# Kernel tuning notes

Measured on AMD Instinct MI355X. Metric: run time of the kernel, lower is better.

The kernel has to match this reference:

```python
import jax, jax.numpy as jnp
import numpy as np

# Config (matches init_kwargs): range [-32,32]^3, voxel 0.5 -> 128^3 grid; BEV 200x200
PC_LOW = np.array([-32.0, -32.0, -32.0], dtype=np.float32)
PC_HIGH = np.array([32.0, 32.0, 32.0], dtype=np.float32)
VOX = 0.5
G = 128
BEV_H, BEV_W = 200, 200
BN_EPS = 1e-5
STRIDES = [1, 2, 1, 2, 1, 1]


def setup_inputs() -> dict:
    key = jax.random.key(0)
    ks = jax.random.split(key, 10)
    N = 2_000_000
    xyz = jax.random.uniform(ks[0], (N, 3), jnp.float32, minval=-32.0, maxval=32.0)
    inten = jax.random.uniform(ks[1], (N, 1), jnp.float32)
    points = jnp.concatenate([xyz, inten], axis=1)  # (N,4)
    chans = [(32, 4), (64, 32), (64, 64), (128, 64), (128, 128), (256, 128)]
    inp = {"points": points}
    for i, (co, ci) in enumerate(chans):
        fan_in = ci * 27
        inp[f"w{i+1}"] = jax.random.normal(ks[2 + i], (co, ci, 3, 3, 3), jnp.float32) / np.sqrt(fan_in)
        inp[f"g{i+1}"] = jnp.ones((co,), jnp.float32)
        inp[f"b{i+1}"] = jnp.zeros((co,), jnp.float32)
    return inp


def _voxelize(points):
    # range filtering + floor-binning + clamp, faithful to voxelize_points (dense path: scatter-ADD)
    low = jnp.asarray(PC_LOW)
    high = jnp.asarray(PC_HIGH)
    mask = jnp.all((points[:, :3] >= low) & (points[:, :3] <= high), axis=1)
    coords = jnp.floor((points[:, :3] - low) / VOX).astype(jnp.int32)
    coords = jnp.clip(coords, 0, G - 1)
    vals = points * mask[:, None].astype(points.dtype)  # invalid points contribute 0
    # original indexes voxel_grid[:, z, y, x]
    grid = jnp.zeros((G, G, G, 4), points.dtype)
    grid = grid.at[coords[:, 2], coords[:, 1], coords[:, 0]].add(vals)
    return jnp.transpose(grid, (3, 0, 1, 2))  # (4, G, G, G)


def _conv3d(x, w, s):
    # PyTorch Conv3d(k=3, padding=1, stride=s), NCDHW
    return jax.lax.conv_general_dilated(
        x, w, window_strides=(s, s, s), padding=[(1, 1), (1, 1), (1, 1)],
        dimension_numbers=("NCDHW", "OIDHW", "NCDHW"))


def _bn_relu(x, g, b):
    # eval-mode BN: running_mean=0, running_var=1
    scale = (g / jnp.sqrt(1.0 + BN_EPS))[None, :, None, None, None]
    return jax.nn.relu(x * scale + b[None, :, None, None, None])


def reference(points, w1, w2, w3, w4, w5, w6,
              g1, g2, g3, g4, g5, g6,
              b1, b2, b3, b4, b5, b6):
    ws = [w1, w2, w3, w4, w5, w6]
    gs = [g1, g2, g3, g4, g5, g6]
    bs = [b1, b2, b3, b4, b5, b6]
    x = _voxelize(points)[None]  # (1,4,G,G,G)
    for w, g, b, s in zip(ws, gs, bs, STRIDES):
        x = _bn_relu(_conv3d(x, w, s), g, b)
    feat = x[0]  # (256, G/4, G/4, G/4)
    bev = jnp.max(feat, axis=2)  # torch.max(..., dim=2) on (C,D1,D2,D3) -> (C,D1,D3)
    # F.interpolate bilinear align_corners=False == jax.image.resize half-pixel bilinear
    bev = jax.image.resize(bev, (bev.shape[0], BEV_H, BEV_W), method="bilinear")
    return bev
```

## Files before the change

### kernel.cpp

```cpp
#include <hip/hip_runtime.h>
#include <hip/hip_fp16.h>
#include <cstdint>
#include <cstddef>

typedef __attribute__((ext_vector_type(8))) short short8;
typedef __attribute__((ext_vector_type(8))) _Float16 half8;
typedef __attribute__((ext_vector_type(16))) float f32x16;

__device__ __forceinline__ float bf2f(unsigned short u) { return __uint_as_float(((unsigned)u) << 16); }
__device__ __forceinline__ unsigned short f2bf(float f) {
    unsigned u = __float_as_uint(f);
    return (unsigned short)((u + 0x7fffu + ((u >> 16) & 1u)) >> 16);
}
__device__ __forceinline__ void sync_lds() {
    asm volatile("s_waitcnt lgkmcnt(0)\n\ts_barrier" ::: "memory");
}

static constexpr float BN_INV = 0.9999950000374997f;

__global__ __launch_bounds__(256) void voxelize_kernel(const float4* __restrict__ pts,
                                                       __half2* __restrict__ grid, int N) {
    int i = blockIdx.x * 256 + threadIdx.x;
    if (i >= N) return;
    float4 p = pts[i];
    if (p.x < -32.f || p.x > 32.f || p.y < -32.f || p.y > 32.f || p.z < -32.f || p.z > 32.f) return;
    int cx = min(max((int)floorf((p.x + 32.f) * 2.f), 0), 127);
    int cy = min(max((int)floorf((p.y + 32.f) * 2.f), 0), 127);
    int cz = min(max((int)floorf((p.z + 32.f) * 2.f), 0), 127);
    int idx = ((((cz + 1) * 130) + (cy + 1)) * 130 + (cx + 1)) * 2;
    unsafeAtomicAdd(&grid[idx],     __floats2half2_rn(p.x, p.y));
    unsafeAtomicAdd(&grid[idx + 1], __floats2half2_rn(p.z, p.w));
}

__global__ __launch_bounds__(256) void repack_w(const float* __restrict__ w, const float* __restrict__ g,
                                                unsigned short* __restrict__ o, int Co, int CI) {
    int i = blockIdx.x * 256 + threadIdx.x;
    int total = 27 * Co * CI;
    if (i >= total) return;
    int ci = i % CI;
    int t = i / CI;
    int co = t % Co;
    int k = t / Co;
    float v = w[((size_t)(co * CI + ci)) * 27 + k] * g[co] * BN_INV;
    o[i] = f2bf(v);
}
__global__ __launch_bounds__(256) void repack_w1m(const float* __restrict__ w, const float* __restrict__ g,
                                                  unsigned short* __restrict__ o) {
    int i = blockIdx.x * 256 + threadIdx.x;
    if (i >= 9 * 32 * 16) return;
    int k16 = i & 15;
    int co = (i >> 4) & 31;
    int p = i >> 9;
    float v = 0.f;
    if (k16 < 12) {
        int dx = k16 >> 2, ci = k16 & 3;
        int dz = p / 3, dy = p % 3;
        v = w[(co * 4 + ci) * 27 + dz * 9 + dy * 3 + dx] * g[co] * BN_INV;
    }
    o[i] = __half_as_ushort(__float2half(v));
}

__global__ __launch_bounds__(256) void conv1_mfma(
    const unsigned short* __restrict__ in, const unsigned short* __restrict__ wa,
    const float* __restrict__ beta, unsigned short* __restrict__ out,
    int zstart, int r0) {
    const int tid = threadIdx.x;
    const int l31 = tid & 31;
    const int lh = (tid >> 5) & 1;
    const int wv = tid >> 6;
    int v = blockIdx.x * 128 + wv * 32 + l31;
    int x = v & 127;
    int y = (v >> 7) & 127;
    int z = zstart + (v >> 14);

    const unsigned short* base = in + ((z * 130 + y) * 130 + x) * 4 + lh * 8;
    uint2 d0[9], d1[9];
    half8 a[9];
#pragma unroll
    for (int p = 0; p < 9; ++p) {
        int dz = p / 3, dy = p % 3;
        const unsigned short* rp = base + (dz * 130 + dy) * 520;
        d0[p] = *(const uint2*)(rp);
        d1[p] = *(const uint2*)(rp + 4);
        a[p] = *(const half8*)(wa + (p * 32 + l31) * 16 + lh * 8);
    }
    f32x16 acc = {0.f};
#pragma unroll
    for (int p = 0; p < 9; ++p) {
        uint4 braw = {d0[p].x, d0[p].y, d1[p].x, d1[p].y};
        half8 b = *(half8*)&braw;
        acc = __builtin_amdgcn_mfma_f32_32x32x16_f16(a[p], b, acc, 0, 0, 0);
    }
    int r = z - zstart + r0;
    int ob = ((r * 130 + (y + 1)) * 130 + (x + 1)) * 32;
#pragma unroll
    for (int g = 0; g < 4; ++g) {
        int cb = 4 * lh + 8 * g;
        float4 bt = *(const float4*)(beta + cb);
        ushort4 u;
        u.x = f2bf(fmaxf(acc[g * 4 + 0] + bt.x, 0.f));
        u.y = f2bf(fmaxf(acc[g * 4 + 1] + bt.y, 0.f));
        u.z = f2bf(fmaxf(acc[g * 4 + 2] + bt.z, 0.f));
        u.w = f2bf(fmaxf(acc[g * 4 + 3] + bt.w, 0.f));
        *(ushort4*)(out + ob + cb) = u;
    }
}

template <int CI, int KC, int S>
__global__ __launch_bounds__(256) void conv_mfma(
    const unsigned short* __restrict__ in, const unsigned short* __restrict__ wb,
    const float* __restrict__ beta, unsigned short* __restrict__ out,
    int D, int lgD, int Xp, int Xpo, int Co, int zin_base, int v_off) {

    constexpr int KCp = KC + 8;
    constexpr int OPB = KC / 8;
    constexpr int NB = KC / 16;
    constexpr int NA = KC / 32;
    constexpr int NCH = KC / 16;
    constexpr int NCC = CI / KC;
    constexpr int STOT = 27 * NCC;

    __shared__ __align__(16) short sA[2 * 64 * KCp];
    __shared__ __align__(16) short sB[2 * 128 * KCp];

    const int tid = threadIdx.x;
    const int l31 = tid & 31;
    const int lh = (tid >> 5) & 1;
    const int wv = tid >> 6;
    const int co0 = blockIdx.x * 64;

    int bgIdx[NB], blB[NB];
#pragma unroll
    for (int j = 0; j < NB; ++j) {
        int idx = tid + j * 256;
        int vL = idx / OPB;
        int oct = idx - vL * OPB;
        int vg = v_off + blockIdx.y * 128 + vL;
        int x = vg & (D - 1);
        int ry = vg >> lgD;
        int y = ry & (D - 1);
        int z = ry >> lgD;
        bgIdx[j] = ((z * S * Xp + y * S) * Xp + x * S) * CI + oct * 8;
        blB[j] = vL * KCp + oct * 8;
    }
    int agIdx[NA], alA[NA];
#pragma unroll
    for (int j = 0; j < NA; ++j) {
        int idx = tid + j * 256;
        int cA = idx / OPB;
        int oct = idx - cA * OPB;
        agIdx[j] = (co0 + cA) * CI + oct * 8;
        alA[j] = cA * KCp + oct * 8;
    }
    const int bfr = (wv * 32 + l31) * KCp + lh * 8;
    const int afr = l31 * KCp + lh * 8;

    short8 rB[2][NB], rA[2][NA];

    auto loadStage = [&](int s, int r) {
        int k = s / NCC;
        int c0 = (s - k * NCC) * KC;
        int dz = k / 9;
        int rr = k - dz * 9;
        int dy = rr / 3;
        int dx = rr - dy * 3;
        int kb = (((dz - zin_base) * Xp + dy) * Xp + dx) * CI + c0;
        int ka = k * Co * CI + c0;
#pragma unroll
        for (int j = 0; j < NB; ++j) rB[r][j] = *(const short8*)(in + bgIdx[j] + kb);
#pragma unroll
        for (int j = 0; j < NA; ++j) rA[r][j] = *(const short8*)(wb + agIdx[j] + ka);
    };
    auto storeLDS = [&](int r, int buf) {
#pragma unroll
        for (int j = 0; j < NB; ++j) *(short8*)(sB + buf * 128 * KCp + blB[j]) = rB[r][j];
#pragma unroll
        for (int j = 0; j < NA; ++j) *(short8*)(sA + buf * 64 * KCp + alA[j]) = rA[r][j];
    };

    f32x16 acc0 = {0.f}, acc1 = {0.f};

    loadStage(0, 0);
    loadStage(1, 1);
    storeLDS(0, 0);
    sync_lds();

#pragma unroll
    for (int s = 0; s < STOT; ++s) {
        if (s + 2 < STOT) loadStage(s + 2, s & 1);
        const short* pB = sB + (s & 1) * 128 * KCp + bfr;
        const short* pA = sA + (s & 1) * 64 * KCp + afr;
#pragma unroll
        for (int c = 0; c < NCH; ++c) {
            short8 bv = *(const short8*)(pB + c * 16);
            short8 a0 = *(const short8*)(pA + c * 16);
            short8 a1 = *(const short8*)(pA + 32 * KCp + c * 16);
            acc0 = __builtin_amdgcn_mfma_f32_32x32x16_bf16(a0, bv, acc0, 0, 0, 0);
            acc1 = __builtin_amdgcn_mfma_f32_32x32x16_bf16(a1, bv, acc1, 0, 0, 0);
        }
        if (s + 1 < STOT) {
            storeLDS((s + 1) & 1, (s + 1) & 1);
            sync_lds();
        }
    }

    int vg = v_off + blockIdx.y * 128 + wv * 32 + l31;
    int x = vg & (D - 1);
    int ry = vg >> lgD;
    int y = ry & (D - 1);
    int z = ry >> lgD;
    size_t ob = (((size_t)(z + 1) * Xpo + (y + 1)) * Xpo + (x + 1)) * Co + co0;
#pragma unroll
    for (int cot = 0; cot < 2; ++cot) {
        const f32x16& a = cot ? acc1 : acc0;
#pragma unroll
        for (int g = 0; g < 4; ++g) {
            int cb = cot * 32 + 4 * lh + 8 * g;
            float4 bt = *(const float4*)(beta + co0 + cb);
            ushort4 u;
            u.x = f2bf(fmaxf(a[g * 4 + 0] + bt.x, 0.f));
            u.y = f2bf(fmaxf(a[g * 4 + 1] + bt.y, 0.f));
            u.z = f2bf(fmaxf(a[g * 4 + 2] + bt.z, 0.f));
            u.w = f2bf(fmaxf(a[g * 4 + 3] + bt.w, 0.f));
            *(ushort4*)(out + ob + cb) = u;
        }
    }
}

__global__ __launch_bounds__(256) void bev_max_kernel(const unsigned short* __restrict__ feat,
                                                      float* __restrict__ bev) {
    int z = blockIdx.x >> 5;
    int x = blockIdx.x & 31;
    int c = threadIdx.x;
    const unsigned short* p = feat + ((((z + 1) * 34) + 1) * 34 + (x + 1)) * 256 + c;
    float mx = 0.f;
#pragma unroll
    for (int y = 0; y < 32; ++y) mx = fmaxf(mx, bf2f(p[y * 34 * 256]));
    bev[(z * 32 + x) * 256 + c] = mx;
}

__global__ __launch_bounds__(256) void resize_kernel(const float* __restrict__ bev,
                                                     float* __restrict__ out) {
    int i = blockIdx.x * 256 + threadIdx.x;
    if (i >= 256 * 200 * 200) return;
    int ox = i % 200;
    int t = i / 200;
    int oy = t % 200;
    int c = t / 200;
    const float sc = 32.0f / 200.0f;
    float fy = (oy + 0.5f) * sc - 0.5f;
    float fx = (ox + 0.5f) * sc - 0.5f;
    float fy0 = floorf(fy), fx0 = floorf(fx);
    float ty = fy - fy0, tx = fx - fx0;
    int y0 = min(max((int)fy0, 0), 31), y1 = min(max((int)fy0 + 1, 0), 31);
    int x0 = min(max((int)fx0, 0), 31), x1 = min(max((int)fx0 + 1, 0), 31);
    float v00 = bev[(y0 * 32 + x0) * 256 + c], v01 = bev[(y0 * 32 + x1) * 256 + c];
    float v10 = bev[(y1 * 32 + x0) * 256 + c], v11 = bev[(y1 * 32 + x1) * 256 + c];
    float top = v00 + tx * (v01 - v00);
    float bot = v10 + tx * (v11 - v10);
    out[i] = top + ty * (bot - top);
}

extern "C" void kernel_launch(void* const* d_in, const int* in_sizes, int n_in,
                              void* d_out, int out_size, void* d_ws, size_t ws_size,
                              hipStream_t stream) {
    const float* points = (const float*)d_in[0];
    int N = in_sizes[0] / 4;
    const float *W[6], *G[6], *B[6];
    for (int i = 0; i < 6; ++i) {
        W[i] = (const float*)d_in[1 + 3 * i];
        G[i] = (const float*)d_in[2 + 3 * i];
        B[i] = (const float*)d_in[3 + 3 * i];
    }

    char* ws = (char*)d_ws;
    const size_t MiB = 1ull << 20;
    unsigned short* gridH = (unsigned short*)(ws);
    unsigned short* O1s = (unsigned short*)(ws + 18 * MiB);
    unsigned short* O2p = (unsigned short*)(ws + 104 * MiB);
    unsigned short* O3p = (unsigned short*)(ws);
    unsigned short* O4p = (unsigned short*)(ws + 37 * MiB);
    unsigned short* O5p = (unsigned short*)(ws + 48 * MiB);
    unsigned short* O6p = (unsigned short*)(ws + 59 * MiB);
    float* bev = (float*)(ws + 80 * MiB);
    unsigned short* wc1 = (unsigned short*)(ws + 140 * MiB);
    unsigned short* wb2 = (unsigned short*)(ws + 140 * MiB + 16384);
    unsigned short* wb3 = wb2 + 27 * 64 * 32;
    unsigned short* wb4 = wb3 + 27 * 64 * 64;
    unsigned short* wb5 = wb4 + 27 * 128 * 64;
    unsigned short* wb6 = wb5 + 27 * 128 * 128;

    repack_w1m<<<18, 256, 0, stream>>>(W[0], G[0], wc1);
    repack_w<<<216, 256, 0, stream>>>(W[1], G[1], wb2, 64, 32);
    repack_w<<<432, 256, 0, stream>>>(W[2], G[2], wb3, 64, 64);
    repack_w<<<864, 256, 0, stream>>>(W[3], G[3], wb4, 128, 64);
    repack_w<<<1728, 256, 0, stream>>>(W[4], G[4], wb5, 128, 128);
    repack_w<<<3456, 256, 0, stream>>>(W[5], G[5], wb6, 256, 128);

    hipMemsetAsync(gridH, 0, 17576000, stream);
    hipMemsetAsync(O2p, 0, 36799488, stream);
    voxelize_kernel<<<(N + 255) / 256, 256, 0, stream>>>((const float4*)points, (__half2*)gridH, N);

    hipMemsetAsync(O1s, 0, 70304000, stream);
    conv1_mfma<<<8192, 256, 0, stream>>>(gridH, wc1, B[0], O1s, 0, 1);
    conv_mfma<32, 32, 2><<<dim3(1, 1024), 256, 0, stream>>>(O1s, wb2, B[1], O2p, 64, 6, 130, 66, 64, 0, 0);
    conv1_mfma<<<8320, 256, 0, stream>>>(gridH, wc1, B[0], O1s, 63, 0);
    conv_mfma<32, 32, 2><<<dim3(1, 1024), 256, 0, stream>>>(O1s, wb2, B[1], O2p, 64, 6, 130, 66, 64, 64, 131072);

    hipMemsetAsync(O3p, 0, 36799488, stream);
    hipMemsetAsync(O4p, 0, 10061824, stream);
    hipMemsetAsync(O5p, 0, 10061824, stream);
    hipMemsetAsync(O6p, 0, 20123648, stream);

    conv_mfma<64, 64, 1><<<dim3(1, 2048), 256, 0, stream>>>(O2p, wb3, B[2], O3p, 64, 6, 66, 66, 64, 0, 0);
    conv_mfma<64, 64, 2><<<dim3(2, 256), 256, 0, stream>>>(O3p, wb4, B[3], O4p, 32, 5, 66, 34, 128, 0, 0);
    conv_mfma<128, 64, 1><<<dim3(2, 256), 256, 0, stream>>>(O4p, wb5, B[4], O5p, 32, 5, 34, 34, 128, 0, 0);
    conv_mfma<128, 64, 1><<<dim3(4, 256), 256, 0, stream>>>(O5p, wb6, B[5], O6p, 32, 5, 34, 34, 256, 0, 0);

    bev_max_kernel<<<1024, 256, 0, stream>>>(O6p, bev);
    resize_kernel<<<40000, 256, 0, stream>>>(bev, (float*)d_out);
}
```

Before: 763.5 us.

## Replace global atomic voxelization with bucket sort and LDS accumulation

Voxelization now runs as four steps: count points per (z, y-quarter) bucket, prefix-scan the counts, scatter the points into bucket order, then accumulate each bucket in fp32 in LDS and write fp16 results to the grid. This removes 4M global fp16 atomics spread across a 17 MB grid and replaces them with LDS atomics plus coalesced writes. In exchange it reads the points twice, writes and reads a 32 MB sorted buffer, and adds kernel launches. The fp32 accumulation also changes rounding compared with the fp16 atomic sums.

```diff
diff --git a/kernel.cpp b/kernel.cpp
--- a/kernel.cpp
+++ b/kernel.cpp
@@ -18,18 +18,114 @@
 
 static constexpr float BN_INV = 0.9999950000374997f;
 
-__global__ __launch_bounds__(256) void voxelize_kernel(const float4* __restrict__ pts,
-                                                       __half2* __restrict__ grid, int N) {
-    int i = blockIdx.x * 256 + threadIdx.x;
-    if (i >= N) return;
-    float4 p = pts[i];
-    if (p.x < -32.f || p.x > 32.f || p.y < -32.f || p.y > 32.f || p.z < -32.f || p.z > 32.f) return;
-    int cx = min(max((int)floorf((p.x + 32.f) * 2.f), 0), 127);
+
+__device__ __forceinline__ int vox_bucket(float4 p, bool& ok) {
+    ok = !(p.x < -32.f || p.x > 32.f || p.y < -32.f || p.y > 32.f || p.z < -32.f || p.z > 32.f);
     int cy = min(max((int)floorf((p.y + 32.f) * 2.f), 0), 127);
     int cz = min(max((int)floorf((p.z + 32.f) * 2.f), 0), 127);
-    int idx = ((((cz + 1) * 130) + (cy + 1)) * 130 + (cx + 1)) * 2;
-    unsafeAtomicAdd(&grid[idx],     __floats2half2_rn(p.x, p.y));
-    unsafeAtomicAdd(&grid[idx + 1], __floats2half2_rn(p.z, p.w));
+    return cz * 4 + (cy >> 5);
+}
+
+__global__ __launch_bounds__(256) void vox_count(const float4* __restrict__ pts,
+                                                 int* __restrict__ cnt, int N) {
+    __shared__ int h[512];
+    for (int t = threadIdx.x; t < 512; t += 256) h[t] = 0;
+    __syncthreads();
+    int stride = gridDim.x * 256;
+    for (int i = blockIdx.x * 256 + threadIdx.x; i < N; i += stride) {
+        float4 p = pts[i];
+        bool ok;
+        int bk = vox_bucket(p, ok);
+        if (ok) atomicAdd(&h[bk], 1);
+    }
+    __syncthreads();
+    for (int t = threadIdx.x; t < 512; t += 256)
+        if (h[t]) atomicAdd(&cnt[t], h[t]);
+}
+
+__global__ void vox_scan(const int* __restrict__ cnt, int* __restrict__ off,
+                         int* __restrict__ cur) {
+    __shared__ int c[512];
+    int t = threadIdx.x;
+    c[t] = cnt[t];
+    __syncthreads();
+    int s = 0;
+    for (int i = 0; i < t; ++i) s += c[i];
+    off[t] = s;
+    cur[t] = s;
+}
+
+__global__ __launch_bounds__(256) void vox_scatter(const float4* __restrict__ pts,
+                                                   int* __restrict__ cur,
+                                                   float4* __restrict__ sorted, int N) {
+    __shared__ int h[512];
+    __shared__ int base[512];
+    int b0 = blockIdx.x * 4096;
+    for (int t = threadIdx.x; t < 512; t += 256) h[t] = 0;
+    __syncthreads();
+    float4 p[16];
+    int bk[16];
+#pragma unroll
+    for (int j = 0; j < 16; ++j) {
+        int i = b0 + j * 256 + threadIdx.x;
+        bk[j] = -1;
+        if (i < N) {
+            p[j] = pts[i];
+            bool ok;
+            int b = vox_bucket(p[j], ok);
+            if (ok) {
+                bk[j] = b;
+                atomicAdd(&h[b], 1);
+            }
+        }
+    }
+    __syncthreads();
+    for (int t = threadIdx.x; t < 512; t += 256) {
+        int n = h[t];
+        base[t] = n ? atomicAdd(&cur[t], n) : 0;
+        h[t] = 0;
+    }
+    __syncthreads();
+#pragma unroll
+    for (int j = 0; j < 16; ++j) {
+        if (bk[j] >= 0) {
+            int r = atomicAdd(&h[bk[j]], 1);
+            sorted[base[bk[j]] + r] = p[j];
+        }
+    }
+}
+
+__global__ __launch_bounds__(256) void vox_accum(const float4* __restrict__ sorted,
+                                                 const int* __restrict__ off,
+                                                 const int* __restrict__ cnt,
+                                                 __half2* __restrict__ grid) {
+    __shared__ float s[32 * 128 * 4];
+    for (int t = threadIdx.x; t < 16384; t += 256) s[t] = 0.f;
+    __syncthreads();
+    int bid = blockIdx.x;
+    int bz = bid >> 2;
+    int ylo = (bid & 3) << 5;
+    int b = off[bid], n = cnt[bid];
+    for (int i = threadIdx.x; i < n; i += 256) {
+        float4 p = sorted[b + i];
+        int cx = min(max((int)floorf((p.x + 32.f) * 2.f), 0), 127);
+        int cy = min(max((int)floorf((p.y + 32.f) * 2.f), 0), 127);
+        float* v = s + ((cy - ylo) * 128 + cx) * 4;
+        unsafeAtomicAdd(v + 0, p.x);
+        unsafeAtomicAdd(v + 1, p.y);
+        unsafeAtomicAdd(v + 2, p.z);
+        unsafeAtomicAdd(v + 3, p.w);
+    }
+    __syncthreads();
+    for (int t = threadIdx.x; t < 4096; t += 256) {
+        int ry = t >> 7, cx = t & 127;
+        const float* v = s + t * 4;
+        union { __half2 h[2]; float2 f; } u;
+        u.h[0] = __floats2half2_rn(v[0], v[1]);
+        u.h[1] = __floats2half2_rn(v[2], v[3]);
+        int gi = (((bz + 1) * 130 + (ylo + ry + 1)) * 130 + (cx + 1)) * 2;
+        *(float2*)(grid + gi) = u.f;
+    }
 }
 
 __global__ __launch_bounds__(256) void repack_w(const float* __restrict__ w, const float* __restrict__ g,
@@ -276,6 +372,10 @@
     char* ws = (char*)d_ws;
     const size_t MiB = 1ull << 20;
     unsigned short* gridH = (unsigned short*)(ws);
+    int* cnt = (int*)(ws + 17580032);
+    int* off = cnt + 512;
+    int* cur = off + 512;
+    float4* sorted = (float4*)(ws + 18 * MiB);
     unsigned short* O1s = (unsigned short*)(ws + 18 * MiB);
     unsigned short* O2p = (unsigned short*)(ws + 104 * MiB);
     unsigned short* O3p = (unsigned short*)(ws);
@@ -298,8 +398,12 @@
     repack_w<<<3456, 256, 0, stream>>>(W[5], G[5], wb6, 256, 128);
 
     hipMemsetAsync(gridH, 0, 17576000, stream);
+    hipMemsetAsync(cnt, 0, 2048, stream);
     hipMemsetAsync(O2p, 0, 36799488, stream);
-    voxelize_kernel<<<(N + 255) / 256, 256, 0, stream>>>((const float4*)points, (__half2*)gridH, N);
+    vox_count<<<1024, 256, 0, stream>>>((const float4*)points, cnt, N);
+    vox_scan<<<1, 512, 0, stream>>>(cnt, off, cur);
+    vox_scatter<<<(N + 4095) / 4096, 256, 0, stream>>>((const float4*)points, cur, sorted, N);
+    vox_accum<<<512, 256, 0, stream>>>(sorted, off, cnt, (__half2*)gridH);
 
     hipMemsetAsync(O1s, 0, 70304000, stream);
     conv1_mfma<<<8192, 256, 0, stream>>>(gridH, wc1, B[0], O1s, 0, 1);
```

After: 686.3 us. 1.11x faster.
